# Optimization experiments

Measured on AMD Instinct MI355X. Metric: run time of the kernel, lower is better.

Reference implementation:

```python
import jax, jax.numpy as jnp
import numpy as np
from jax import lax

TF_ALPHA = 0.125


def _teacher_force(z, x, alpha):
    # z: (B, dz), x: (B, dx); force first dx dims of z where x is not NaN
    dx = x.shape[-1]
    head = z[:, :dx]
    forced = jnp.where(jnp.isnan(x), head, alpha * x + (1.0 - alpha) * head)
    return jnp.concatenate([forced, z[:, dx:]], axis=-1)


def setup_inputs() -> dict:
    key = jax.random.key(0)
    ks = jax.random.split(key, 8)
    B, T, dx, dz, dh, ds = 256, 1024, 64, 128, 512, 16
    X = jax.random.normal(ks[0], (B, T, dx), dtype=jnp.float32)
    inputs = jax.random.normal(ks[1], (B, T, ds), dtype=jnp.float32)
    # A in (0, 0.9) for stable linear part; small weight scales to avoid blowup over T steps
    A = jax.random.uniform(ks[2], (B, dz), dtype=jnp.float32) * 0.9
    W1 = jax.random.normal(ks[3], (B, dz, dh), dtype=jnp.float32) * (0.5 / np.sqrt(dh))
    W2 = jax.random.normal(ks[4], (B, dh, dz), dtype=jnp.float32) * (0.5 / np.sqrt(dz))
    h1 = jax.random.normal(ks[5], (B, dz), dtype=jnp.float32) * 0.1
    h2 = jax.random.normal(ks[6], (B, dh), dtype=jnp.float32) * 0.1
    C = jax.random.normal(ks[7], (B, dz, ds), dtype=jnp.float32) * (0.5 / np.sqrt(ds))
    return {"X": X, "inputs": inputs, "A": A, "W1": W1, "W2": W2,
            "h1": h1, "h2": h2, "C": C}


def _plrnn_forward(X, inputs, A, W1, W2, h1, h2, C):
    B, T, dx = X.shape
    dz = A.shape[-1]
    # z0 = zeros teacher-forced with alpha=1 from X[:, 0]
    z0 = jnp.zeros((B, dz), dtype=X.dtype)
    z0 = _teacher_force(z0, X[:, 0], alpha=1.0)

    Xt = jnp.transpose(X, (1, 0, 2))        # (T, B, dx)
    St = jnp.transpose(inputs, (1, 0, 2))   # (T, B, ds)

    def step(z, xs):
        x_t, s_t = xs
        zf = _teacher_force(z, x_t, TF_ALPHA)
        pre = jnp.einsum('bhz,bz->bh', W2, zf) + h2          # (B, dh)
        z_new = (A * zf
                 + jnp.einsum('bzh,bh->bz', W1, jax.nn.relu(pre))
                 + h1
                 + jnp.einsum('bzs,bs->bz', C, s_t))
        return z_new, z_new

    _, Z = lax.scan(step, z0, (Xt, St))      # Z: (T, B, dz)
    Z = jnp.transpose(Z, (1, 0, 2))          # (B, T, dz)
    return Z[:, :, :dx]                      # dim_x_proj == 0 path


def reference(X, inputs, A, W1, W2, h1, h2, C):
    return _plrnn_forward(X, inputs, A, W1, W2, h1, h2, C)
```

## Files before the change

kernel.cpp:

```cpp
#include <hip/hip_runtime.h>
#include <math.h>


#define NB 256
#define T  1024
#define DX 64
#define DZ 128
#define DH 512
#define DS 16
#define CHUNK 128

typedef _Float16 half8 __attribute__((ext_vector_type(8)));
typedef _Float16 v4h   __attribute__((ext_vector_type(4)));
typedef float    f32x4 __attribute__((ext_vector_type(4)));

__device__ __forceinline__ half8 cvt8(const float* __restrict__ src) {
  const float4 a = *reinterpret_cast<const float4*>(src);
  const float4 c = *reinterpret_cast<const float4*>(src + 4);
  half8 h;
  h[0] = (_Float16)a.x; h[1] = (_Float16)a.y; h[2] = (_Float16)a.z; h[3] = (_Float16)a.w;
  h[4] = (_Float16)c.x; h[5] = (_Float16)c.y; h[6] = (_Float16)c.z; h[7] = (_Float16)c.w;
  return h;
}

__global__ __launch_bounds__(512, 2) void plrnn_kernel(
    const float* __restrict__ X, const float* __restrict__ S,
    const float* __restrict__ A, const float* __restrict__ W1,
    const float* __restrict__ W2, const float* __restrict__ h1,
    const float* __restrict__ h2, const float* __restrict__ C,
    float* __restrict__ out)
{
  __shared__ __align__(16) _Float16 zf_h[DZ];
  __shared__ __align__(16) _Float16 rt[544];
  __shared__ __align__(16) float    Xc[CHUNK][DX];
  __shared__ __align__(16) float    Sc[CHUNK][DS];
  __shared__ __align__(16) float    outc[CHUNK][DX];

  const int b   = blockIdx.x;
  const int tid = threadIdx.x;
  const int w   = tid >> 6;
  const int l   = tid & 63;
  const int g   = l >> 4;
  const int r15 = l & 15;

  {
    #pragma unroll
    for (int k = 0; k < 4; ++k) {
      const int flat = k * 2048 + tid * 4;
      int srow = 1 + (flat >> 6);
      if (srow > T - 1) srow = T - 1;
      const float4 v = *reinterpret_cast<const float4*>(X + ((size_t)b * T + srow) * DX + (flat & 63));
      *reinterpret_cast<float4*>(&((float*)Xc)[flat]) = v;
    }
    const int flat = tid * 4;
    const float4 v = *reinterpret_cast<const float4*>(S + ((size_t)b * T) * DS + flat);
    *reinterpret_cast<float4*>(&((float*)Sc)[flat]) = v;
  }

  if (tid < 16) rt[528 + tid] = (tid == 0) ? (_Float16)1.0f : (_Float16)0.0f;

  half8 w2f[4][4];
  #pragma unroll
  for (int mt = 0; mt < 4; ++mt)
    #pragma unroll
    for (int kt = 0; kt < 4; ++kt)
      w2f[mt][kt] = cvt8(W2 + ((size_t)b * DH + 64 * w + 16 * mt + r15) * DZ + 32 * kt + 8 * g);

  half8 w1f[16];
  #pragma unroll
  for (int kt = 0; kt < 16; ++kt)
    w1f[kt] = cvt8(W1 + ((size_t)b * DZ + 16 * w + r15) * DH + 32 * kt + 8 * g);
  half8 w1ft;
  #pragma unroll
  for (int e = 0; e < 8; ++e) w1ft[e] = (_Float16)0.0f;
  if (g == 0)      w1ft = cvt8(C + ((size_t)b * DZ + 16 * w + r15) * DS + 0);
  else if (g == 1) w1ft = cvt8(C + ((size_t)b * DZ + 16 * w + r15) * DS + 8);
  else if (g == 2) w1ft[0] = (_Float16)h1[(size_t)b * DZ + 16 * w + r15];

  f32x4 h2v[4];
  #pragma unroll
  for (int mt = 0; mt < 4; ++mt)
    h2v[mt] = *reinterpret_cast<const f32x4*>(h2 + (size_t)b * DH + 64 * w + 16 * mt + 4 * g);

  f32x4 Areg = {0.f, 0.f, 0.f, 0.f};
  f32x4 zfcur = {0.f, 0.f, 0.f, 0.f};
  if (r15 == 0) {
    Areg = *reinterpret_cast<const f32x4*>(A + (size_t)b * DZ + 16 * w + 4 * g);
    if (w < 4) {
      const f32x4 x0 = *reinterpret_cast<const f32x4*>(X + ((size_t)b * T) * DX + 16 * w + 4 * g);
      #pragma unroll
      for (int j = 0; j < 4; ++j) {
        const float x = x0[j];
        const float z0 = (x != x) ? 0.f : x;
        zfcur[j] = (x != x) ? z0 : (0.125f * x + 0.875f * z0);
      }
    }
    v4h zp;
    #pragma unroll
    for (int j = 0; j < 4; ++j) zp[j] = (_Float16)zfcur[j];
    *reinterpret_cast<v4h*>(&zf_h[16 * w + 4 * g]) = zp;
  }
  __syncthreads();

  const f32x4 zero4 = {0.f, 0.f, 0.f, 0.f};

  for (int t = 0; t < T; ++t) {
    if ((t & (CHUNK - 1)) == 0 && t) {
      const int c0 = t - CHUNK;
      #pragma unroll
      for (int k = 0; k < 4; ++k) {
        const int flat = k * 2048 + tid * 4;
        const float4 v = *reinterpret_cast<const float4*>(&((float*)outc)[flat]);
        *reinterpret_cast<float4*>(out + ((size_t)b * T + c0) * DX + flat) = v;
      }
      #pragma unroll
      for (int k = 0; k < 4; ++k) {
        const int flat = k * 2048 + tid * 4;
        int srow = t + 1 + (flat >> 6);
        if (srow > T - 1) srow = T - 1;
        const float4 v = *reinterpret_cast<const float4*>(X + ((size_t)b * T + srow) * DX + (flat & 63));
        *reinterpret_cast<float4*>(&((float*)Xc)[flat]) = v;
      }
      const int flat = tid * 4;
      const float4 v = *reinterpret_cast<const float4*>(S + ((size_t)b * T + t) * DS + flat);
      *reinterpret_cast<float4*>(&((float*)Sc)[flat]) = v;
      __syncthreads();
    }
    const int tc = t & (CHUNK - 1);

    half8 bz[4];
    #pragma unroll
    for (int kt = 0; kt < 4; ++kt)
      bz[kt] = *reinterpret_cast<const half8*>(zf_h + 32 * kt + 8 * g);

    f32x4 acc1[4];
    #pragma unroll
    for (int mt = 0; mt < 4; ++mt) acc1[mt] = h2v[mt];
    #pragma unroll
    for (int kt = 0; kt < 4; ++kt)
      #pragma unroll
      for (int mt = 0; mt < 4; ++mt)
        acc1[mt] = __builtin_amdgcn_mfma_f32_16x16x32_f16(w2f[mt][kt], bz[kt], acc1[mt], 0, 0, 0);

    if (r15 == 0) {
      #pragma unroll
      for (int mt = 0; mt < 4; ++mt) {
        v4h p;
        p.x = (_Float16)fmaxf(acc1[mt][0], 0.f);
        p.y = (_Float16)fmaxf(acc1[mt][1], 0.f);
        p.z = (_Float16)fmaxf(acc1[mt][2], 0.f);
        p.w = (_Float16)fmaxf(acc1[mt][3], 0.f);
        *reinterpret_cast<v4h*>(&rt[64 * w + 16 * mt + 4 * g]) = p;
      }
    }
    if (tid < 16) rt[512 + tid] = (_Float16)Sc[tc][tid];
    __syncthreads();

    f32x4 acc2[4];
    #pragma unroll
    for (int i = 0; i < 4; ++i) acc2[i] = zero4;
    #pragma unroll
    for (int kt = 0; kt < 16; ++kt) {
      const half8 br = *reinterpret_cast<const half8*>(rt + 32 * kt + 8 * g);
      acc2[kt & 3] = __builtin_amdgcn_mfma_f32_16x16x32_f16(w1f[kt], br, acc2[kt & 3], 0, 0, 0);
    }
    {
      const half8 br = *reinterpret_cast<const half8*>(rt + 512 + 8 * g);
      acc2[0] = __builtin_amdgcn_mfma_f32_16x16x32_f16(w1ft, br, acc2[0], 0, 0, 0);
    }

    if (r15 == 0) {
      const f32x4 u = (acc2[0] + acc2[1]) + (acc2[2] + acc2[3]);
      f32x4 zn, zfn;
      #pragma unroll
      for (int j = 0; j < 4; ++j) zn[j] = Areg[j] * zfcur[j] + u[j];
      zfn = zn;
      if (w < 4) {
        *reinterpret_cast<f32x4*>(&outc[tc][16 * w + 4 * g]) = zn;
        const f32x4 xv = *reinterpret_cast<const f32x4*>(&Xc[tc][16 * w + 4 * g]);
        #pragma unroll
        for (int j = 0; j < 4; ++j) {
          const float x = xv[j];
          zfn[j] = (x != x) ? zn[j] : (0.125f * x + 0.875f * zn[j]);
        }
      }
      zfcur = zfn;
      v4h zp;
      #pragma unroll
      for (int j = 0; j < 4; ++j) zp[j] = (_Float16)zfn[j];
      *reinterpret_cast<v4h*>(&zf_h[16 * w + 4 * g]) = zp;
    }
    __syncthreads();
  }

  {
    const int c0 = T - CHUNK;
    #pragma unroll
    for (int k = 0; k < 4; ++k) {
      const int flat = k * 2048 + tid * 4;
      const float4 v = *reinterpret_cast<const float4*>(&((float*)outc)[flat]);
      *reinterpret_cast<float4*>(out + ((size_t)b * T + c0) * DX + flat) = v;
    }
  }
}

extern "C" void kernel_launch(void* const* d_in, const int* in_sizes, int n_in,
                              void* d_out, int out_size, void* d_ws, size_t ws_size,
                              hipStream_t stream) {
  const float* X  = (const float*)d_in[0];
  const float* S  = (const float*)d_in[1];
  const float* A  = (const float*)d_in[2];
  const float* W1 = (const float*)d_in[3];
  const float* W2 = (const float*)d_in[4];
  const float* h1 = (const float*)d_in[5];
  const float* h2 = (const float*)d_in[6];
  const float* C  = (const float*)d_in[7];
  float* out = (float*)d_out;
  plrnn_kernel<<<dim3(NB), dim3(512), 0, stream>>>(X, S, A, W1, W2, h1, h2, C, out);
}
```

Before: 1.030 ms.

## Split W1 matvec along hidden dim per wave with cross-wave partial-sum reduction

```diff
diff --git a/kernel.cpp b/kernel.cpp
--- a/kernel.cpp
+++ b/kernel.cpp
@@ -21,6 +21,34 @@
   h[0] = (_Float16)a.x; h[1] = (_Float16)a.y; h[2] = (_Float16)a.z; h[3] = (_Float16)a.w;
   h[4] = (_Float16)c.x; h[5] = (_Float16)c.y; h[6] = (_Float16)c.z; h[7] = (_Float16)c.w;
   return h;
+}
+
+__device__ __forceinline__ f32x4 sel4(int c, f32x4 a, f32x4 b) {
+  f32x4 r;
+  r[0] = c ? a[0] : b[0];  r[1] = c ? a[1] : b[1];
+  r[2] = c ? a[2] : b[2];  r[3] = c ? a[3] : b[3];
+  return r;
+}
+
+template <int CTRL>
+__device__ __forceinline__ f32x4 dpp_xor_add(f32x4 v) {
+  f32x4 r;
+  #pragma unroll
+  for (int j = 0; j < 4; ++j) {
+    const int t = __builtin_amdgcn_update_dpp(0, __float_as_int(v[j]), CTRL, 0xF, 0xF, true);
+    r[j] = v[j] + __int_as_float(t);
+  }
+  return r;
+}
+
+__device__ __forceinline__ f32x4 swz_xor4_add(f32x4 v) {
+  f32x4 r;
+  #pragma unroll
+  for (int j = 0; j < 4; ++j) {
+    const int t = __builtin_amdgcn_ds_swizzle(__float_as_int(v[j]), 0x101F);
+    r[j] = v[j] + __int_as_float(t);
+  }
+  return r;
 }
 
 __global__ __launch_bounds__(512, 2) void plrnn_kernel(
@@ -32,6 +60,7 @@
 {
   __shared__ __align__(16) _Float16 zf_h[DZ];
   __shared__ __align__(16) _Float16 rt[544];
+  __shared__ __align__(16) float    part[8][132];
   __shared__ __align__(16) float    Xc[CHUNK][DX];
   __shared__ __align__(16) float    Sc[CHUNK][DS];
   __shared__ __align__(16) float    outc[CHUNK][DX];
@@ -42,6 +71,7 @@
   const int l   = tid & 63;
   const int g   = l >> 4;
   const int r15 = l & 15;
+  const int zb  = (l >> 3) & 3;
 
   {
     #pragma unroll
@@ -66,39 +96,45 @@
     for (int kt = 0; kt < 4; ++kt)
       w2f[mt][kt] = cvt8(W2 + ((size_t)b * DH + 64 * w + 16 * mt + r15) * DZ + 32 * kt + 8 * g);
 
-  half8 w1f[16];
-  #pragma unroll
-  for (int kt = 0; kt < 16; ++kt)
-    w1f[kt] = cvt8(W1 + ((size_t)b * DZ + 16 * w + r15) * DH + 32 * kt + 8 * g);
-  half8 w1ft;
-  #pragma unroll
-  for (int e = 0; e < 8; ++e) w1ft[e] = (_Float16)0.0f;
-  if (g == 0)      w1ft = cvt8(C + ((size_t)b * DZ + 16 * w + r15) * DS + 0);
-  else if (g == 1) w1ft = cvt8(C + ((size_t)b * DZ + 16 * w + r15) * DS + 8);
-  else if (g == 2) w1ft[0] = (_Float16)h1[(size_t)b * DZ + 16 * w + r15];
+  half8 w1f[8][2];
+  #pragma unroll
+  for (int mt = 0; mt < 8; ++mt)
+    #pragma unroll
+    for (int kt = 0; kt < 2; ++kt)
+      w1f[mt][kt] = cvt8(W1 + ((size_t)b * DZ + 16 * mt + r15) * DH + 64 * w + 32 * kt + 8 * g);
+
+  half8 w1ft[8];
+  #pragma unroll
+  for (int mt = 0; mt < 8; ++mt)
+    #pragma unroll
+    for (int e = 0; e < 8; ++e) w1ft[mt][e] = (_Float16)0.0f;
+  if (w == 0) {
+    #pragma unroll
+    for (int mt = 0; mt < 8; ++mt) {
+      const int row = 16 * mt + r15;
+      if (g == 0)      w1ft[mt] = cvt8(C + ((size_t)b * DZ + row) * DS + 0);
+      else if (g == 1) w1ft[mt] = cvt8(C + ((size_t)b * DZ + row) * DS + 8);
+      else if (g == 2) w1ft[mt][0] = (_Float16)h1[(size_t)b * DZ + row];
+    }
+  }
 
   f32x4 h2v[4];
   #pragma unroll
   for (int mt = 0; mt < 4; ++mt)
     h2v[mt] = *reinterpret_cast<const f32x4*>(h2 + (size_t)b * DH + 64 * w + 16 * mt + 4 * g);
 
-  f32x4 Areg = {0.f, 0.f, 0.f, 0.f};
+  const f32x4 Areg = *reinterpret_cast<const f32x4*>(A + (size_t)b * DZ + 16 * w + 4 * zb);
   f32x4 zfcur = {0.f, 0.f, 0.f, 0.f};
-  if (r15 == 0) {
-    Areg = *reinterpret_cast<const f32x4*>(A + (size_t)b * DZ + 16 * w + 4 * g);
-    if (w < 4) {
-      const f32x4 x0 = *reinterpret_cast<const f32x4*>(X + ((size_t)b * T) * DX + 16 * w + 4 * g);
-      #pragma unroll
-      for (int j = 0; j < 4; ++j) {
-        const float x = x0[j];
-        const float z0 = (x != x) ? 0.f : x;
-        zfcur[j] = (x != x) ? z0 : (0.125f * x + 0.875f * z0);
-      }
-    }
+  if (w < 4) {
+    const f32x4 x0 = *reinterpret_cast<const f32x4*>(X + ((size_t)b * T) * DX + 16 * w + 4 * zb);
+    #pragma unroll
+    for (int j = 0; j < 4; ++j) zfcur[j] = (x0[j] != x0[j]) ? 0.f : x0[j];
+  }
+  if (l < 32 && (l & 7) == 0) {
     v4h zp;
     #pragma unroll
     for (int j = 0; j < 4; ++j) zp[j] = (_Float16)zfcur[j];
-    *reinterpret_cast<v4h*>(&zf_h[16 * w + 4 * g]) = zp;
+    *reinterpret_cast<v4h*>(&zf_h[16 * w + 4 * zb]) = zp;
   }
   __syncthreads();
 
@@ -128,6 +164,14 @@
     }
     const int tc = t & (CHUNK - 1);
 
+    if (w == 0 && l < 4) {
+      const f32x4 sv = *reinterpret_cast<const f32x4*>(&Sc[tc][4 * l]);
+      v4h sp;
+      #pragma unroll
+      for (int j = 0; j < 4; ++j) sp[j] = (_Float16)sv[j];
+      *reinterpret_cast<v4h*>(&rt[512 + 4 * l]) = sp;
+    }
+
     half8 bz[4];
     #pragma unroll
     for (int kt = 0; kt < 4; ++kt)
@@ -135,60 +179,81 @@
 
     f32x4 acc1[4];
     #pragma unroll
-    for (int mt = 0; mt < 4; ++mt) acc1[mt] = h2v[mt];
-    #pragma unroll
-    for (int kt = 0; kt < 4; ++kt)
+    for (int mt = 0; mt < 4; ++mt)
+      acc1[mt] = __builtin_amdgcn_mfma_f32_16x16x32_f16(w2f[mt][0], bz[0], h2v[mt], 0, 0, 0);
+    #pragma unroll
+    for (int kt = 1; kt < 4; ++kt)
       #pragma unroll
       for (int mt = 0; mt < 4; ++mt)
         acc1[mt] = __builtin_amdgcn_mfma_f32_16x16x32_f16(w2f[mt][kt], bz[kt], acc1[mt], 0, 0, 0);
 
-    if (r15 == 0) {
-      #pragma unroll
-      for (int mt = 0; mt < 4; ++mt) {
+    {
+      const f32x4 lo = sel4(r15 & 1, acc1[1], acc1[0]);
+      const f32x4 hi = sel4(r15 & 1, acc1[3], acc1[2]);
+      const f32x4 sv = sel4(r15 & 2, hi, lo);
+      if (r15 < 4) {
         v4h p;
-        p.x = (_Float16)fmaxf(acc1[mt][0], 0.f);
-        p.y = (_Float16)fmaxf(acc1[mt][1], 0.f);
-        p.z = (_Float16)fmaxf(acc1[mt][2], 0.f);
-        p.w = (_Float16)fmaxf(acc1[mt][3], 0.f);
-        *reinterpret_cast<v4h*>(&rt[64 * w + 16 * mt + 4 * g]) = p;
+        #pragma unroll
+        for (int j = 0; j < 4; ++j) p[j] = (_Float16)fmaxf(sv[j], 0.f);
+        *reinterpret_cast<v4h*>(&rt[64 * w + 16 * r15 + 4 * g]) = p;
       }
     }
-    if (tid < 16) rt[512 + tid] = (_Float16)Sc[tc][tid];
+
+    half8 br[2];
+    #pragma unroll
+    for (int kt = 0; kt < 2; ++kt)
+      br[kt] = *reinterpret_cast<const half8*>(rt + 64 * w + 32 * kt + 8 * g);
+
+    f32x4 acc2[8];
+    #pragma unroll
+    for (int mt = 0; mt < 8; ++mt)
+      acc2[mt] = __builtin_amdgcn_mfma_f32_16x16x32_f16(w1f[mt][0], br[0], zero4, 0, 0, 0);
+    #pragma unroll
+    for (int mt = 0; mt < 8; ++mt)
+      acc2[mt] = __builtin_amdgcn_mfma_f32_16x16x32_f16(w1f[mt][1], br[1], acc2[mt], 0, 0, 0);
+    if (w == 0) {
+      const half8 brt = *reinterpret_cast<const half8*>(rt + 512 + 8 * g);
+      #pragma unroll
+      for (int mt = 0; mt < 8; ++mt)
+        acc2[mt] = __builtin_amdgcn_mfma_f32_16x16x32_f16(w1ft[mt], brt, acc2[mt], 0, 0, 0);
+    }
+
+    {
+      const f32x4 s01 = sel4(r15 & 1, acc2[1], acc2[0]);
+      const f32x4 s23 = sel4(r15 & 1, acc2[3], acc2[2]);
+      const f32x4 s45 = sel4(r15 & 1, acc2[5], acc2[4]);
+      const f32x4 s67 = sel4(r15 & 1, acc2[7], acc2[6]);
+      const f32x4 a03 = sel4(r15 & 2, s23, s01);
+      const f32x4 a47 = sel4(r15 & 2, s67, s45);
+      const f32x4 sv  = sel4(r15 & 4, a47, a03);
+      if (r15 < 8)
+        *reinterpret_cast<f32x4*>(&part[w][16 * r15 + 4 * g]) = sv;
+    }
     __syncthreads();
 
-    f32x4 acc2[4];
-    #pragma unroll
-    for (int i = 0; i < 4; ++i) acc2[i] = zero4;
-    #pragma unroll
-    for (int kt = 0; kt < 16; ++kt) {
-      const half8 br = *reinterpret_cast<const half8*>(rt + 32 * kt + 8 * g);
-      acc2[kt & 3] = __builtin_amdgcn_mfma_f32_16x16x32_f16(w1f[kt], br, acc2[kt & 3], 0, 0, 0);
-    }
-    {
-      const half8 br = *reinterpret_cast<const half8*>(rt + 512 + 8 * g);
-      acc2[0] = __builtin_amdgcn_mfma_f32_16x16x32_f16(w1ft, br, acc2[0], 0, 0, 0);
-    }
-
-    if (r15 == 0) {
-      const f32x4 u = (acc2[0] + acc2[1]) + (acc2[2] + acc2[3]);
-      f32x4 zn, zfn;
-      #pragma unroll
-      for (int j = 0; j < 4; ++j) zn[j] = Areg[j] * zfcur[j] + u[j];
-      zfn = zn;
-      if (w < 4) {
-        *reinterpret_cast<f32x4*>(&outc[tc][16 * w + 4 * g]) = zn;
-        const f32x4 xv = *reinterpret_cast<const f32x4*>(&Xc[tc][16 * w + 4 * g]);
-        #pragma unroll
-        for (int j = 0; j < 4; ++j) {
-          const float x = xv[j];
-          zfn[j] = (x != x) ? zn[j] : (0.125f * x + 0.875f * zn[j]);
-        }
-      }
-      zfcur = zfn;
+    f32x4 u = *reinterpret_cast<const f32x4*>(&part[l & 7][16 * w + 4 * zb]);
+    u = dpp_xor_add<0xB1>(u);
+    u = dpp_xor_add<0x4E>(u);
+    u = swz_xor4_add(u);
+
+    f32x4 zn, zfn;
+    #pragma unroll
+    for (int j = 0; j < 4; ++j) zn[j] = Areg[j] * zfcur[j] + u[j];
+    zfn = zn;
+    if (w < 4) {
+      const f32x4 xv = *reinterpret_cast<const f32x4*>(&Xc[tc][16 * w + 4 * zb]);
+      #pragma unroll
+      for (int j = 0; j < 4; ++j)
+        zfn[j] = (xv[j] != xv[j]) ? zn[j] : (0.125f * xv[j] + 0.875f * zn[j]);
+      if (l < 32 && (l & 7) == 0)
+        *reinterpret_cast<f32x4*>(&outc[tc][16 * w + 4 * zb]) = zn;
+    }
+    zfcur = zfn;
+    if (l < 32 && (l & 7) == 0) {
       v4h zp;
       #pragma unroll
       for (int j = 0; j < 4; ++j) zp[j] = (_Float16)zfn[j];
-      *reinterpret_cast<v4h*>(&zf_h[16 * w + 4 * g]) = zp;
+      *reinterpret_cast<v4h*>(&zf_h[16 * w + 4 * zb]) = zp;
     }
     __syncthreads();
   }
```

Measured after the change: 1.087 ms. 5.5% more time.

## Overlap own-wave W1 MFMAs before barrier and hoist S/C/h1 tail off critical path

Applied to the files above, without the earlier changes.

```diff
diff --git a/kernel.cpp b/kernel.cpp
--- a/kernel.cpp
+++ b/kernel.cpp
@@ -31,7 +31,7 @@
     float* __restrict__ out)
 {
   __shared__ __align__(16) _Float16 zf_h[DZ];
-  __shared__ __align__(16) _Float16 rt[544];
+  __shared__ __align__(16) _Float16 rt[DH];
   __shared__ __align__(16) float    Xc[CHUNK][DX];
   __shared__ __align__(16) float    Sc[CHUNK][DS];
   __shared__ __align__(16) float    outc[CHUNK][DX];
@@ -57,8 +57,6 @@
     *reinterpret_cast<float4*>(&((float*)Sc)[flat]) = v;
   }
 
-  if (tid < 16) rt[528 + tid] = (tid == 0) ? (_Float16)1.0f : (_Float16)0.0f;
-
   half8 w2f[4][4];
   #pragma unroll
   for (int mt = 0; mt < 4; ++mt)
@@ -68,32 +66,34 @@
 
   half8 w1f[16];
   #pragma unroll
-  for (int kt = 0; kt < 16; ++kt)
-    w1f[kt] = cvt8(W1 + ((size_t)b * DZ + 16 * w + r15) * DH + 32 * kt + 8 * g);
+  for (int j = 0; j < 16; ++j) {
+    const int kt = (2 * w + j) & 15;
+    w1f[j] = cvt8(W1 + ((size_t)b * DZ + 16 * w + r15) * DH + 32 * kt + 8 * g);
+  }
+
   half8 w1ft;
   #pragma unroll
   for (int e = 0; e < 8; ++e) w1ft[e] = (_Float16)0.0f;
-  if (g == 0)      w1ft = cvt8(C + ((size_t)b * DZ + 16 * w + r15) * DS + 0);
-  else if (g == 1) w1ft = cvt8(C + ((size_t)b * DZ + 16 * w + r15) * DS + 8);
-  else if (g == 2) w1ft[0] = (_Float16)h1[(size_t)b * DZ + 16 * w + r15];
+  {
+    const int row = 16 * w + r15;
+    if (g == 0)      w1ft = cvt8(C + ((size_t)b * DZ + row) * DS + 0);
+    else if (g == 1) w1ft = cvt8(C + ((size_t)b * DZ + row) * DS + 8);
+  }
 
   f32x4 h2v[4];
   #pragma unroll
   for (int mt = 0; mt < 4; ++mt)
     h2v[mt] = *reinterpret_cast<const f32x4*>(h2 + (size_t)b * DH + 64 * w + 16 * mt + 4 * g);
 
-  f32x4 Areg = {0.f, 0.f, 0.f, 0.f};
+  f32x4 Areg = {0.f, 0.f, 0.f, 0.f}, h1reg = {0.f, 0.f, 0.f, 0.f};
   f32x4 zfcur = {0.f, 0.f, 0.f, 0.f};
   if (r15 == 0) {
-    Areg = *reinterpret_cast<const f32x4*>(A + (size_t)b * DZ + 16 * w + 4 * g);
+    Areg  = *reinterpret_cast<const f32x4*>(A  + (size_t)b * DZ + 16 * w + 4 * g);
+    h1reg = *reinterpret_cast<const f32x4*>(h1 + (size_t)b * DZ + 16 * w + 4 * g);
     if (w < 4) {
       const f32x4 x0 = *reinterpret_cast<const f32x4*>(X + ((size_t)b * T) * DX + 16 * w + 4 * g);
       #pragma unroll
-      for (int j = 0; j < 4; ++j) {
-        const float x = x0[j];
-        const float z0 = (x != x) ? 0.f : x;
-        zfcur[j] = (x != x) ? z0 : (0.125f * x + 0.875f * z0);
-      }
+      for (int j = 0; j < 4; ++j) zfcur[j] = (x0[j] != x0[j]) ? 0.f : x0[j];
     }
     v4h zp;
     #pragma unroll
@@ -121,12 +121,25 @@
         const float4 v = *reinterpret_cast<const float4*>(X + ((size_t)b * T + srow) * DX + (flat & 63));
         *reinterpret_cast<float4*>(&((float*)Xc)[flat]) = v;
       }
-      const int flat = tid * 4;
-      const float4 v = *reinterpret_cast<const float4*>(S + ((size_t)b * T + t) * DS + flat);
-      *reinterpret_cast<float4*>(&((float*)Sc)[flat]) = v;
+      {
+        const int flat = tid * 4;
+        const float4 v = *reinterpret_cast<const float4*>(S + ((size_t)b * T + t) * DS + flat);
+        *reinterpret_cast<float4*>(&((float*)Sc)[flat]) = v;
+      }
       __syncthreads();
     }
     const int tc = t & (CHUNK - 1);
+
+    const f32x4 xv  = *reinterpret_cast<const f32x4*>(&Xc[tc][16 * (w & 3) + 4 * g]);
+    const f32x4 sa0 = *reinterpret_cast<const f32x4*>(&Sc[tc][8 * (g & 1)]);
+    const f32x4 sa1 = *reinterpret_cast<const f32x4*>(&Sc[tc][8 * (g & 1) + 4]);
+    half8 brt;
+    #pragma unroll
+    for (int e = 0; e < 4; ++e) {
+      brt[e]     = (g < 2) ? (_Float16)sa0[e] : (_Float16)0.0f;
+      brt[e + 4] = (g < 2) ? (_Float16)sa1[e] : (_Float16)0.0f;
+    }
+    const f32x4 tailv = __builtin_amdgcn_mfma_f32_16x16x32_f16(w1ft, brt, zero4, 0, 0, 0);
 
     half8 bz[4];
     #pragma unroll
@@ -135,9 +148,10 @@
 
     f32x4 acc1[4];
     #pragma unroll
-    for (int mt = 0; mt < 4; ++mt) acc1[mt] = h2v[mt];
-    #pragma unroll
-    for (int kt = 0; kt < 4; ++kt)
+    for (int mt = 0; mt < 4; ++mt)
+      acc1[mt] = __builtin_amdgcn_mfma_f32_16x16x32_f16(w2f[mt][0], bz[0], h2v[mt], 0, 0, 0);
+    #pragma unroll
+    for (int kt = 1; kt < 4; ++kt)
       #pragma unroll
       for (int mt = 0; mt < 4; ++mt)
         acc1[mt] = __builtin_amdgcn_mfma_f32_16x16x32_f16(w2f[mt][kt], bz[kt], acc1[mt], 0, 0, 0);
@@ -146,49 +160,53 @@
       #pragma unroll
       for (int mt = 0; mt < 4; ++mt) {
         v4h p;
-        p.x = (_Float16)fmaxf(acc1[mt][0], 0.f);
-        p.y = (_Float16)fmaxf(acc1[mt][1], 0.f);
-        p.z = (_Float16)fmaxf(acc1[mt][2], 0.f);
-        p.w = (_Float16)fmaxf(acc1[mt][3], 0.f);
+        p[0] = (_Float16)fmaxf(acc1[mt][0], 0.f);
+        p[1] = (_Float16)fmaxf(acc1[mt][1], 0.f);
+        p[2] = (_Float16)fmaxf(acc1[mt][2], 0.f);
+        p[3] = (_Float16)fmaxf(acc1[mt][3], 0.f);
         *reinterpret_cast<v4h*>(&rt[64 * w + 16 * mt + 4 * g]) = p;
       }
     }
-    if (tid < 16) rt[512 + tid] = (_Float16)Sc[tc][tid];
+
+    f32x4 acc2[8];
+    {
+      const half8 br0 = *reinterpret_cast<const half8*>(rt + 64 * w + 8 * g);
+      const half8 br1 = *reinterpret_cast<const half8*>(rt + 64 * w + 32 + 8 * g);
+      acc2[0] = __builtin_amdgcn_mfma_f32_16x16x32_f16(w1f[0], br0, tailv, 0, 0, 0);
+      acc2[1] = __builtin_amdgcn_mfma_f32_16x16x32_f16(w1f[1], br1, zero4, 0, 0, 0);
+    }
     __syncthreads();
 
-    f32x4 acc2[4];
-    #pragma unroll
-    for (int i = 0; i < 4; ++i) acc2[i] = zero4;
-    #pragma unroll
-    for (int kt = 0; kt < 16; ++kt) {
-      const half8 br = *reinterpret_cast<const half8*>(rt + 32 * kt + 8 * g);
-      acc2[kt & 3] = __builtin_amdgcn_mfma_f32_16x16x32_f16(w1f[kt], br, acc2[kt & 3], 0, 0, 0);
-    }
-    {
-      const half8 br = *reinterpret_cast<const half8*>(rt + 512 + 8 * g);
-      acc2[0] = __builtin_amdgcn_mfma_f32_16x16x32_f16(w1ft, br, acc2[0], 0, 0, 0);
+    #pragma unroll
+    for (int j = 2; j < 8; ++j) {
+      const half8 br = *reinterpret_cast<const half8*>(rt + 32 * ((2 * w + j) & 15) + 8 * g);
+      acc2[j] = __builtin_amdgcn_mfma_f32_16x16x32_f16(w1f[j], br, zero4, 0, 0, 0);
+    }
+    #pragma unroll
+    for (int j = 8; j < 16; ++j) {
+      const half8 br = *reinterpret_cast<const half8*>(rt + 32 * ((2 * w + j) & 15) + 8 * g);
+      acc2[j - 8] = __builtin_amdgcn_mfma_f32_16x16x32_f16(w1f[j], br, acc2[j - 8], 0, 0, 0);
     }
 
     if (r15 == 0) {
-      const f32x4 u = (acc2[0] + acc2[1]) + (acc2[2] + acc2[3]);
+      const f32x4 u = ((acc2[0] + acc2[1]) + (acc2[2] + acc2[3]))
+                    + ((acc2[4] + acc2[5]) + (acc2[6] + acc2[7]));
       f32x4 zn, zfn;
       #pragma unroll
-      for (int j = 0; j < 4; ++j) zn[j] = Areg[j] * zfcur[j] + u[j];
+      for (int j = 0; j < 4; ++j) zn[j] = Areg[j] * zfcur[j] + u[j] + h1reg[j];
       zfn = zn;
       if (w < 4) {
-        *reinterpret_cast<f32x4*>(&outc[tc][16 * w + 4 * g]) = zn;
-        const f32x4 xv = *reinterpret_cast<const f32x4*>(&Xc[tc][16 * w + 4 * g]);
         #pragma unroll
-        for (int j = 0; j < 4; ++j) {
-          const float x = xv[j];
-          zfn[j] = (x != x) ? zn[j] : (0.125f * x + 0.875f * zn[j]);
-        }
+        for (int j = 0; j < 4; ++j)
+          zfn[j] = (xv[j] != xv[j]) ? zn[j] : (0.125f * xv[j] + 0.875f * zn[j]);
       }
       zfcur = zfn;
       v4h zp;
       #pragma unroll
       for (int j = 0; j < 4; ++j) zp[j] = (_Float16)zfn[j];
       *reinterpret_cast<v4h*>(&zf_h[16 * w + 4 * g]) = zp;
+      if (w < 4)
+        *reinterpret_cast<f32x4*>(&outc[tc][16 * w + 4 * g]) = zn;
     }
     __syncthreads();
   }
```

Measured after the change: 1.157 ms. +12.3%, slower.
